# Optimization experiments

Measured on AMD Instinct MI355X. Metric: run time of the kernel, lower is better.

## Reference

```python
import jax, jax.numpy as jnp
import numpy as np

H = 256   # input_size
P = 256   # state_size
BATCH, L = 8, 4096
DT_MIN, DT_MAX = 1e-3, 1e-1
LN_EPS = 1e-5


def _hippo_params():
    # HiPPO-N matrix (num_blocks=1), eigendecomposition in numpy (float64 then cast)
    idx = np.arange(P, dtype=np.float64)
    s = np.sqrt(idx + 0.5)
    A = -np.outer(s, s)
    A = np.tril(A) - np.triu(A, 1)
    np.fill_diagonal(A, -0.5)
    ev, V = np.linalg.eig(A)
    order = np.argsort(ev.real)
    ev, V = ev[order], V[:, order]
    return ev, V


def setup_inputs() -> dict:
    key = jax.random.key(0)
    k_u, = jax.random.split(key, 1)
    ev, V = _hippo_params()
    rng = np.random.default_rng(0)
    log_lambda_real = np.log(-np.clip(ev.real, None, -1e-4)).astype(np.float32)
    lambda_imag = ev.imag.astype(np.float32)
    V_inv = np.linalg.inv(V)
    B_init = rng.standard_normal((P, H)) / np.sqrt(P)
    B_tilde = V_inv @ B_init.astype(np.complex128)
    C_init = rng.standard_normal((H, P)) / np.sqrt(P)
    C_tilde = C_init.astype(np.complex128) @ V
    log_delta = (rng.random(P) * (np.log(DT_MAX) - np.log(DT_MIN)) + np.log(DT_MIN)).astype(np.float32)
    return {
        "u": jax.random.normal(k_u, (BATCH, L, H), dtype=jnp.float32),
        "log_lambda_real": jnp.asarray(log_lambda_real),
        "lambda_imag": jnp.asarray(lambda_imag),
        "B_tilde_real": jnp.asarray(B_tilde.real, dtype=jnp.float32),
        "B_tilde_imag": jnp.asarray(B_tilde.imag, dtype=jnp.float32),
        "C_tilde_real": jnp.asarray(C_tilde.real, dtype=jnp.float32),
        "C_tilde_imag": jnp.asarray(C_tilde.imag, dtype=jnp.float32),
        "log_delta": jnp.asarray(log_delta),
        "gamma": jnp.ones((H,), dtype=jnp.float32),
        "beta": jnp.zeros((H,), dtype=jnp.float32),
    }


def _layernorm(x, gamma, beta):
    mu = jnp.mean(x, axis=-1, keepdims=True)
    var = jnp.mean(jnp.square(x - mu), axis=-1, keepdims=True)
    return (x - mu) * jax.lax.rsqrt(var + LN_EPS) * gamma + beta


def _ssm(h, log_lambda_real, lambda_imag, B_tilde_real, B_tilde_imag,
         C_tilde_real, C_tilde_imag, log_delta):
    # Continuous-time diagonal SSM params
    lam = -jnp.exp(log_lambda_real) + 1j * lambda_imag            # (P,) complex
    B_tilde = B_tilde_real + 1j * B_tilde_imag                     # (P,H)
    C_tilde = C_tilde_real + 1j * C_tilde_imag                     # (H,P)
    delta = jnp.exp(log_delta)                                     # (P,)
    # ZOH discretization (eq. 6 of the S5 paper)
    lambda_bar = jnp.exp(lam * delta)                              # (P,)
    B_bar = ((lambda_bar - 1.0) / lam)[:, None] * B_tilde          # (P,H)
    # Bu_k = B_bar @ u_k  ->  (B,L,P) complex
    Bu = jnp.einsum('blh,ph->blp', h.astype(jnp.complex64), B_bar.astype(jnp.complex64))
    # Parallel associative scan for x_k = lambda_bar * x_{k-1} + Bu_k
    a = jnp.broadcast_to(lambda_bar.astype(jnp.complex64), Bu.shape)
    def combine(c1, c2):
        a1, b1 = c1
        a2, b2 = c2
        return a1 * a2, a2 * b1 + b2
    _, xs = jax.lax.associative_scan(combine, (a, Bu), axis=1)     # (B,L,P)
    # Project back to real output: y = Re(C_tilde @ x)
    y = jnp.einsum('blp,hp->blh', xs, C_tilde.astype(jnp.complex64)).real
    return y


def reference(u, log_lambda_real, lambda_imag, B_tilde_real, B_tilde_imag,
              C_tilde_real, C_tilde_imag, log_delta, gamma, beta):
    # S5Block: pre-LayerNorm -> S5 SSM -> GELU -> residual
    h = _layernorm(u, gamma, beta)
    y = _ssm(h, log_lambda_real, lambda_imag, B_tilde_real, B_tilde_imag,
             C_tilde_real, C_tilde_imag, log_delta)
    return u + jax.nn.gelu(y)
```

## Files before the change

### kernel.cpp

```cpp
#include <hip/hip_runtime.h>
#include <math.h>

#define HDIM 256
#define PDIM 256
#define BATCH 8
#define LSEQ 4096
#define MTOT (BATCH * LSEQ)
#define NCHUNK 128
#define CHLEN 32

typedef __attribute__((ext_vector_type(8))) short bf16x8;
typedef __attribute__((ext_vector_type(4))) float f32x4;

__device__ __forceinline__ unsigned short f2bf(float f) {
    union { float f; unsigned int u; } v; v.f = f;
    unsigned int r = v.u + 0x7FFFu + ((v.u >> 16) & 1u);
    return (unsigned short)(r >> 16);
}
__device__ __forceinline__ float bf2f(unsigned int lo16) {
    union { unsigned int u; float f; } v; v.u = lo16 << 16;
    return v.f;
}

__device__ __forceinline__ void gload_lds16(const void* g, void* l) {
    __builtin_amdgcn_global_load_lds(
        (const __attribute__((address_space(1))) void*)g,
        (__attribute__((address_space(3))) void*)l, 16, 0, 0);
}

__global__ void wpack_k(const float* __restrict__ llr, const float* __restrict__ lim,
                        const float* __restrict__ ldl,
                        const float* __restrict__ Br, const float* __restrict__ Bi,
                        const float* __restrict__ Cr, const float* __restrict__ Ci,
                        unsigned short* __restrict__ W1t, unsigned short* __restrict__ W2t,
                        float* __restrict__ par) {
    int h = threadIdx.x;
    if (blockIdx.x < PDIM) {
        int p = blockIdx.x;
        float er = expf(llr[p]);
        float im = lim[p];
        float d  = expf(ldl[p]);
        float zr = -er * d, zi = im * d;
        float ea = expf(zr);
        float sz, cz; sincosf(zi, &sz, &cz);
        float ar = ea * cz, ai = ea * sz;
        float dr = -er, di = im;
        float den = dr * dr + di * di;
        float nr = ar - 1.0f, ni = ai;
        float cr = (nr * dr + ni * di) / den;
        float ci = (ni * dr - nr * di) / den;
        float br = Br[p * HDIM + h], bi = Bi[p * HDIM + h];
        W1t[(2 * p) * HDIM + h]     = f2bf(cr * br - ci * bi);
        W1t[(2 * p + 1) * HDIM + h] = f2bf(cr * bi + ci * br);
    } else if (blockIdx.x < 2 * PDIM) {
        int p = blockIdx.x - PDIM;
        W2t[h * (2 * PDIM) + 2 * p]     = f2bf(Cr[h * PDIM + p]);
        W2t[h * (2 * PDIM) + 2 * p + 1] = f2bf(-Ci[h * PDIM + p]);
    } else {
        int p = h;
        float er = expf(llr[p]);
        float im = lim[p];
        float d  = expf(ldl[p]);
        float zr = -er * d, zi = im * d;
        float ea = expf(zr);
        float sz, cz; sincosf(zi, &sz, &cz);
        float ar = ea * cz, ai = ea * sz;
        float dr = -er, di = im;
        float den = dr * dr + di * di;
        float nr = ar - 1.0f, ni = ai;
        float cr = (nr * dr + ni * di) / den;
        float ci = (ni * dr - nr * di) / den;
        float eC = expf((float)CHLEN * zr);
        float sC, cC;
        sincosf((float)CHLEN * zi, &sC, &cC);
        par[2 * p]            = ar;
        par[2 * p + 1]        = ai;
        par[512 + 2 * p]      = cr;
        par[512 + 2 * p + 1]  = ci;
        par[1024 + 2 * p]     = eC * cC;
        par[1024 + 2 * p + 1] = eC * sC;
    }
}

__global__ void ln_k(const float* __restrict__ u, unsigned short* __restrict__ hbf,
                     const float* __restrict__ gamma, const float* __restrict__ beta) {
    __shared__ float gS[HDIM], bS[HDIM];
    int t = threadIdx.x;
    gS[t] = gamma[t]; bS[t] = beta[t];
    int lane = t & 63, wv = t >> 6;
    int row = blockIdx.x * 4 + wv;
    float4 v = *(const float4*)(u + (size_t)row * HDIM + lane * 4);
    float s  = v.x + v.y + v.z + v.w;
    float sq = v.x * v.x + v.y * v.y + v.z * v.z + v.w * v.w;
    #pragma unroll
    for (int o = 1; o < 64; o <<= 1) { s += __shfl_xor(s, o); sq += __shfl_xor(sq, o); }
    float mu = s * (1.0f / HDIM);
    float rs = rsqrtf(sq * (1.0f / HDIM) - mu * mu + 1e-5f);
    __syncthreads();
    int c = lane * 4;
    ushort4 o;
    o.x = f2bf((v.x - mu) * rs * gS[c + 0] + bS[c + 0]);
    o.y = f2bf((v.y - mu) * rs * gS[c + 1] + bS[c + 1]);
    o.z = f2bf((v.z - mu) * rs * gS[c + 2] + bS[c + 2]);
    o.w = f2bf((v.w - mu) * rs * gS[c + 3] + bS[c + 3]);
    *(ushort4*)(hbf + (size_t)row * HDIM + c) = o;
}

template <int MODE, int K>
__launch_bounds__(256, 2)
__global__ void mfma_gemm_k(const unsigned short* __restrict__ A,
                            const unsigned short* __restrict__ B,
                            void* __restrict__ outv,
                            const float* __restrict__ u,
                            int N) {
    __shared__ __align__(16) unsigned short As[2][128 * 32];
    __shared__ __align__(16) unsigned short Bs[2][128 * 32];
    const int t = threadIdx.x;

    const int nbn  = (int)gridDim.x;
    const int flat = (int)blockIdx.y * nbn + (int)blockIdx.x;
    const int nwg  = nbn * (int)gridDim.y;
    const int tile = (flat & 7) * (nwg >> 3) + (flat >> 3);
    const int bn = tile % nbn, bm = tile / nbn;

    const int lane = t & 63, w = t >> 6;

    const int srow   = 32 * w + (lane >> 2);
    const int schunk = (lane & 3) ^ ((lane >> 3) & 3);
    const unsigned short* gA = A + (size_t)(bm * 128 + srow) * K + schunk * 8;
    const unsigned short* gB = B + (size_t)(bn * 128 + srow) * K + schunk * 8;
    const int l0 = (32 * w) * 32;
    const int l1 = (32 * w + 16) * 32;

    const int wm = (w & 1) * 64;
    const int wn = (w >> 1) * 64;
    const int mrow = lane & 15;
    const int rsw  = (mrow >> 1) & 3;
    const int cch  = lane >> 4;
    const int fcol = ((cch ^ rsw) * 8);

    f32x4 acc[4][4] = {};
    constexpr int NT = K / 32;

    gload_lds16(gA,          &As[0][l0]);
    gload_lds16(gA + 16 * K, &As[0][l1]);
    gload_lds16(gB,          &Bs[0][l0]);
    gload_lds16(gB + 16 * K, &Bs[0][l1]);

    #pragma unroll
    for (int tt = 0; tt < NT; ++tt) {
        const int cur = tt & 1;
        if (tt + 1 < NT) {
            const int k0 = (tt + 1) * 32;
            gload_lds16(gA + k0,          &As[cur ^ 1][l0]);
            gload_lds16(gA + 16 * K + k0, &As[cur ^ 1][l1]);
            gload_lds16(gB + k0,          &Bs[cur ^ 1][l0]);
            gload_lds16(gB + 16 * K + k0, &Bs[cur ^ 1][l1]);
            asm volatile("s_waitcnt vmcnt(4)" ::: "memory");
        } else {
            asm volatile("s_waitcnt vmcnt(0)" ::: "memory");
        }
        __builtin_amdgcn_sched_barrier(0);
        __builtin_amdgcn_s_barrier();
        __builtin_amdgcn_sched_barrier(0);

        bf16x8 fa[4], fb[4];
        #pragma unroll
        for (int i = 0; i < 4; i++) {
            fa[i] = *(const bf16x8*)&As[cur][(wm + i * 16 + mrow) * 32 + fcol];
            fb[i] = *(const bf16x8*)&Bs[cur][(wn + i * 16 + mrow) * 32 + fcol];
        }
        __builtin_amdgcn_s_setprio(1);
        #pragma unroll
        for (int i = 0; i < 4; i++)
            #pragma unroll
            for (int j = 0; j < 4; j++)
                acc[i][j] = __builtin_amdgcn_mfma_f32_16x16x32_bf16(fa[i], fb[j], acc[i][j], 0, 0, 0);
        __builtin_amdgcn_s_setprio(0);
        __builtin_amdgcn_sched_barrier(0);
        if (tt + 1 < NT) __builtin_amdgcn_s_barrier();
    }

    const int r0 = (lane >> 4) * 4;
    const int c0 = lane & 15;
    #pragma unroll
    for (int i = 0; i < 4; i++) {
        #pragma unroll
        for (int r = 0; r < 4; r++) {
            const size_t rowoff = (size_t)(bm * 128 + wm + i * 16 + r0 + r) * N;
            #pragma unroll
            for (int j = 0; j < 4; j++) {
                const int col_g = bn * 128 + wn + j * 16 + c0;
                float y = acc[i][j][r];
                if (MODE == 0) {
                    ((unsigned short*)outv)[rowoff + col_g] = f2bf(y);
                } else {
                    float z = 0.7978845608f * fmaf(0.044715f * y * y, y, y);
                    float e = __expf(2.0f * z);
                    float th = 1.0f - 2.0f / (e + 1.0f);
                    float g = 0.5f * y * (1.0f + th);
                    ((float*)outv)[rowoff + col_g] = u[rowoff + col_g] + g;
                }
            }
        }
    }
}

__global__ void scan_reduce_k(const unsigned short* __restrict__ Bu,
                              const float* __restrict__ par, float* __restrict__ last) {
    int t = threadIdx.x;
    int lane = t & 63, g = t >> 6;
    int c = blockIdx.x * 4 + g, b = blockIdx.y;
    int p0 = lane * 4;
    float4 a01 = *(const float4*)(par + 2 * p0);
    float4 a23 = *(const float4*)(par + 2 * p0 + 4);
    float ar[4] = {a01.x, a01.z, a23.x, a23.z};
    float ai[4] = {a01.y, a01.w, a23.y, a23.w};
    float xr[4] = {0.f, 0.f, 0.f, 0.f}, xi[4] = {0.f, 0.f, 0.f, 0.f};
    const uint4* q = (const uint4*)(Bu + ((size_t)b * LSEQ + (size_t)c * CHLEN) * 512) + lane;
    #pragma unroll 8
    for (int j = 0; j < CHLEN; j++) {
        uint4 v = q[(size_t)j * 64];
        unsigned int vv[4] = {v.x, v.y, v.z, v.w};
        #pragma unroll
        for (int k = 0; k < 4; k++) {
            float vr = bf2f(vv[k] & 0xFFFFu), vi = bf2f(vv[k] >> 16);
            float nr = fmaf(ar[k], xr[k], fmaf(-ai[k], xi[k], vr));
            float ni = fmaf(ar[k], xi[k], fmaf(ai[k], xr[k], vi));
            xr[k] = nr; xi[k] = ni;
        }
    }
    float* lp = last + ((size_t)b * NCHUNK + c) * 512 + 2 * p0;
    *(float4*)lp       = make_float4(xr[0], xi[0], xr[1], xi[1]);
    *(float4*)(lp + 4) = make_float4(xr[2], xi[2], xr[3], xi[3]);
}

__global__ void scan_carry_k(const float* __restrict__ last, float* __restrict__ prefix,
                             const float* __restrict__ par) {
    int p = threadIdx.x, b = blockIdx.x;
    float Ar = par[1024 + 2 * p], Ai = par[1024 + 2 * p + 1];
    float Pr = 0.0f, Pi = 0.0f;
    const float2* lp = (const float2*)(last + (size_t)b * NCHUNK * 512) + p;
    float2* pp = (float2*)(prefix + (size_t)b * NCHUNK * 512) + p;
    for (int c0 = 0; c0 < NCHUNK; c0 += 16) {
        float2 v[16];
        #pragma unroll
        for (int j = 0; j < 16; j++) v[j] = lp[(size_t)(c0 + j) * 256];
        #pragma unroll
        for (int j = 0; j < 16; j++) {
            pp[(size_t)(c0 + j) * 256] = make_float2(Pr, Pi);
            float nr = fmaf(Ar, Pr, fmaf(-Ai, Pi, v[j].x));
            float ni = fmaf(Ar, Pi, fmaf(Ai, Pr, v[j].y));
            Pr = nr; Pi = ni;
        }
    }
}

__global__ void scan_apply_k(unsigned short* __restrict__ Bu, const float* __restrict__ par,
                             const float* __restrict__ prefix) {
    int t = threadIdx.x;
    int lane = t & 63, g = t >> 6;
    int c = blockIdx.x * 4 + g, b = blockIdx.y;
    int p0 = lane * 4;
    float4 a01 = *(const float4*)(par + 2 * p0);
    float4 a23 = *(const float4*)(par + 2 * p0 + 4);
    float ar[4] = {a01.x, a01.z, a23.x, a23.z};
    float ai[4] = {a01.y, a01.w, a23.y, a23.w};
    const float* pf = prefix + ((size_t)b * NCHUNK + c) * 512 + 2 * p0;
    float4 P01 = *(const float4*)pf;
    float4 P23 = *(const float4*)(pf + 4);
    float xr[4] = {P01.x, P01.z, P23.x, P23.z};
    float xi[4] = {P01.y, P01.w, P23.y, P23.w};
    uint4* q = (uint4*)(Bu + ((size_t)b * LSEQ + (size_t)c * CHLEN) * 512) + lane;
    #pragma unroll 8
    for (int j = 0; j < CHLEN; j++) {
        uint4 v = q[(size_t)j * 64];
        unsigned int vv[4] = {v.x, v.y, v.z, v.w};
        #pragma unroll
        for (int k = 0; k < 4; k++) {
            float vr = bf2f(vv[k] & 0xFFFFu), vi = bf2f(vv[k] >> 16);
            float nr = fmaf(ar[k], xr[k], fmaf(-ai[k], xi[k], vr));
            float ni = fmaf(ar[k], xi[k], fmaf(ai[k], xr[k], vi));
            xr[k] = nr; xi[k] = ni;
            vv[k] = (unsigned int)f2bf(nr) | ((unsigned int)f2bf(ni) << 16);
        }
        uint4 o; o.x = vv[0]; o.y = vv[1]; o.z = vv[2]; o.w = vv[3];
        q[(size_t)j * 64] = o;
    }
}

extern "C" void kernel_launch(void* const* d_in, const int* in_sizes, int n_in,
                              void* d_out, int out_size, void* d_ws, size_t ws_size,
                              hipStream_t stream) {
    const float* u   = (const float*)d_in[0];
    const float* llr = (const float*)d_in[1];
    const float* lim = (const float*)d_in[2];
    const float* Br  = (const float*)d_in[3];
    const float* Bi  = (const float*)d_in[4];
    const float* Cr  = (const float*)d_in[5];
    const float* Ci  = (const float*)d_in[6];
    const float* ldl = (const float*)d_in[7];
    const float* gam = (const float*)d_in[8];
    const float* bet = (const float*)d_in[9];
    float* out = (float*)d_out;

    float* ws     = (float*)d_ws;
    float* par    = ws;
    float* last   = ws + 2048;
    float* prefix = last + (size_t)BATCH * NCHUNK * 512;
    unsigned short* W1t = (unsigned short*)(prefix + (size_t)BATCH * NCHUNK * 512);
    unsigned short* W2t = W1t + 512 * HDIM;
    unsigned short* hbf = W2t + HDIM * 512;
    unsigned short* Bu  = hbf + (size_t)MTOT * HDIM;

    ln_k<<<MTOT / 4, 256, 0, stream>>>(u, hbf, gam, bet);
    wpack_k<<<2 * PDIM + 1, HDIM, 0, stream>>>(llr, lim, ldl, Br, Bi, Cr, Ci, W1t, W2t, par);

    mfma_gemm_k<0, HDIM><<<dim3(512 / 128, MTOT / 128), 256, 0, stream>>>(
        hbf, W1t, (void*)Bu, nullptr, 512);

    scan_reduce_k<<<dim3(NCHUNK / 4, BATCH), 256, 0, stream>>>(Bu, par, last);
    scan_carry_k<<<BATCH, PDIM, 0, stream>>>(last, prefix, par);
    scan_apply_k<<<dim3(NCHUNK / 4, BATCH), 256, 0, stream>>>(Bu, par, prefix);

    mfma_gemm_k<1, 512><<<dim3(HDIM / 128, MTOT / 128), 256, 0, stream>>>(
        Bu, W2t, (void*)out, u, HDIM);
}
```

Baseline: 163.6 us.

## Fuse scan apply into output GEMM with chunk states kept in LDS

Replaces the separate scan-apply pass, which rewrote Bu in global memory, and the second GEMM with one kernel. Each block takes one 32-row chunk, applies the carried prefix to recompute the states into swizzled LDS, then runs a bf16 MFMA GEMM against W2t with double-buffered weight loads. GELU and the residual add are applied in the epilogue. This removes a full global write and reread of Bu, at the cost of an M-tile of only 32 rows, which gives less weight reuse, and a large LDS footprint per block.

```diff
diff --git a/kernel.cpp b/kernel.cpp
--- a/kernel.cpp
+++ b/kernel.cpp
@@ -256,36 +256,104 @@
     }
 }
 
-__global__ void scan_apply_k(unsigned short* __restrict__ Bu, const float* __restrict__ par,
-                             const float* __restrict__ prefix) {
-    int t = threadIdx.x;
-    int lane = t & 63, g = t >> 6;
-    int c = blockIdx.x * 4 + g, b = blockIdx.y;
-    int p0 = lane * 4;
-    float4 a01 = *(const float4*)(par + 2 * p0);
-    float4 a23 = *(const float4*)(par + 2 * p0 + 4);
-    float ar[4] = {a01.x, a01.z, a23.x, a23.z};
-    float ai[4] = {a01.y, a01.w, a23.y, a23.w};
-    const float* pf = prefix + ((size_t)b * NCHUNK + c) * 512 + 2 * p0;
-    float4 P01 = *(const float4*)pf;
-    float4 P23 = *(const float4*)(pf + 4);
-    float xr[4] = {P01.x, P01.z, P23.x, P23.z};
-    float xi[4] = {P01.y, P01.w, P23.y, P23.w};
-    uint4* q = (uint4*)(Bu + ((size_t)b * LSEQ + (size_t)c * CHLEN) * 512) + lane;
-    #pragma unroll 8
-    for (int j = 0; j < CHLEN; j++) {
-        uint4 v = q[(size_t)j * 64];
-        unsigned int vv[4] = {v.x, v.y, v.z, v.w};
-        #pragma unroll
-        for (int k = 0; k < 4; k++) {
-            float vr = bf2f(vv[k] & 0xFFFFu), vi = bf2f(vv[k] >> 16);
-            float nr = fmaf(ar[k], xr[k], fmaf(-ai[k], xi[k], vr));
-            float ni = fmaf(ar[k], xi[k], fmaf(ai[k], xr[k], vi));
-            xr[k] = nr; xi[k] = ni;
-            vv[k] = (unsigned int)f2bf(nr) | ((unsigned int)f2bf(ni) << 16);
-        }
-        uint4 o; o.x = vv[0]; o.y = vv[1]; o.z = vv[2]; o.w = vv[3];
-        q[(size_t)j * 64] = o;
+__launch_bounds__(256, 2)
+__global__ void apply_gemm2_k(const unsigned short* __restrict__ Bu,
+                              const float* __restrict__ par,
+                              const float* __restrict__ prefix,
+                              const unsigned short* __restrict__ W2t,
+                              const float* __restrict__ u, float* __restrict__ out) {
+    __shared__ __align__(16) unsigned short Xs[32 * 512];
+    __shared__ __align__(16) unsigned short Bs[2][256 * 32];
+    const int t = threadIdx.x;
+    const int lane = t & 63, w = t >> 6;
+    const int c = blockIdx.x, b = blockIdx.y;
+    const size_t row0 = (size_t)b * LSEQ + (size_t)c * CHLEN;
+
+    const int schunk = (lane & 3) ^ ((lane >> 3) & 3);
+    const unsigned short* gW = W2t + (size_t)(w * 64 + (lane >> 2)) * 512 + schunk * 8;
+
+    #pragma unroll
+    for (int m = 0; m < 4; m++)
+        gload_lds16(gW + (size_t)m * 16 * 512, &Bs[0][(w * 64 + m * 16) * 32]);
+
+    {
+        const unsigned int* q = (const unsigned int*)(Bu + row0 * 512) + t;
+        unsigned int vv[32];
+        #pragma unroll
+        for (int j = 0; j < 32; j++) vv[j] = q[(size_t)j * 256];
+        const float2 P = ((const float2*)(prefix + ((size_t)b * NCHUNK + c) * 512))[t];
+        const float ar = par[2 * t], ai = par[2 * t + 1];
+        float xr = P.x, xi = P.y;
+        #pragma unroll
+        for (int j = 0; j < 32; j++) {
+            float vr = bf2f(vv[j] & 0xFFFFu), vi = bf2f(vv[j] >> 16);
+            float nr = fmaf(ar, xr, fmaf(-ai, xi, vr));
+            float ni = fmaf(ar, xi, fmaf(ai, xr, vi));
+            xr = nr; xi = ni;
+            unsigned int pk = (unsigned int)f2bf(xr) | ((unsigned int)f2bf(xi) << 16);
+            *(unsigned int*)&Xs[j * 512 + ((((t >> 2) ^ (j & 7)) << 3) + (t & 3) * 2)] = pk;
+        }
+    }
+
+    const int mrow = lane & 15;
+    const int rsw  = (mrow >> 1) & 3;
+    const int cch  = lane >> 4;
+    const int fcol = (cch ^ rsw) * 8;
+
+    f32x4 acc[2][4] = {};
+    __syncthreads();
+
+    #pragma unroll
+    for (int tt = 0; tt < 16; tt++) {
+        const int cur = tt & 1;
+        if (tt + 1 < 16) {
+            const int k0 = (tt + 1) * 32;
+            #pragma unroll
+            for (int m = 0; m < 4; m++)
+                gload_lds16(gW + (size_t)m * 16 * 512 + k0,
+                            &Bs[cur ^ 1][(w * 64 + m * 16) * 32]);
+            asm volatile("s_waitcnt vmcnt(4)" ::: "memory");
+        } else {
+            asm volatile("s_waitcnt vmcnt(0)" ::: "memory");
+        }
+        __builtin_amdgcn_sched_barrier(0);
+
+        bf16x8 fa[2], fb[4];
+        #pragma unroll
+        for (int i = 0; i < 2; i++) {
+            const int r = i * 16 + mrow;
+            fa[i] = *(const bf16x8*)&Xs[r * 512 + (((tt * 4 + cch) ^ (r & 7)) << 3)];
+        }
+        #pragma unroll
+        for (int j = 0; j < 4; j++)
+            fb[j] = *(const bf16x8*)&Bs[cur][(w * 64 + j * 16 + mrow) * 32 + fcol];
+        __builtin_amdgcn_s_setprio(1);
+        #pragma unroll
+        for (int i = 0; i < 2; i++)
+            #pragma unroll
+            for (int j = 0; j < 4; j++)
+                acc[i][j] = __builtin_amdgcn_mfma_f32_16x16x32_bf16(fa[i], fb[j], acc[i][j], 0, 0, 0);
+        __builtin_amdgcn_s_setprio(0);
+        __builtin_amdgcn_sched_barrier(0);
+    }
+
+    const int r0 = (lane >> 4) * 4, c0 = lane & 15;
+    #pragma unroll
+    for (int i = 0; i < 2; i++) {
+        #pragma unroll
+        for (int r = 0; r < 4; r++) {
+            const size_t rowoff = (row0 + i * 16 + r0 + r) * HDIM;
+            #pragma unroll
+            for (int j = 0; j < 4; j++) {
+                const int col = w * 64 + j * 16 + c0;
+                float y = acc[i][j][r];
+                float z = 0.7978845608f * fmaf(0.044715f * y * y, y, y);
+                float e = __expf(2.0f * z);
+                float th = 1.0f - 2.0f / (e + 1.0f);
+                float g = 0.5f * y * (1.0f + th);
+                out[rowoff + col] = u[rowoff + col] + g;
+            }
+        }
     }
 }
 
@@ -321,8 +389,6 @@
 
     scan_reduce_k<<<dim3(NCHUNK / 4, BATCH), 256, 0, stream>>>(Bu, par, last);
     scan_carry_k<<<BATCH, PDIM, 0, stream>>>(last, prefix, par);
-    scan_apply_k<<<dim3(NCHUNK / 4, BATCH), 256, 0, stream>>>(Bu, par, prefix);
-
-    mfma_gemm_k<1, 512><<<dim3(HDIM / 128, MTOT / 128), 256, 0, stream>>>(
-        Bu, W2t, (void*)out, u, HDIM);
-}
+
+    apply_gemm2_k<<<dim3(NCHUNK, BATCH), 256, 0, stream>>>(Bu, par, prefix, W2t, u, out);
+}
```

Result: no change. 163.2 us (-0.3%).
